# Kernel tuning notes

Hardware: AMD Instinct MI355X
Metric: run time of the kernel (lower is better)

The kernel has to match this reference:

```python
import jax, jax.numpy as jnp
import numpy as np

B, S, D = 8, 1024, 768
H = 12
DH = D // H  # 64


def setup_inputs() -> dict:
    key = jax.random.key(0)
    k1, k2 = jax.random.split(key)
    x = jax.random.normal(k1, (B, S, D), dtype=jnp.float32)
    attention_mask = jnp.zeros((B, 1, 1, S), dtype=jnp.float32)
    W = jax.random.normal(k2, (D, D), dtype=jnp.float32) * (1.0 / np.sqrt(D))
    b = jnp.zeros((D,), dtype=jnp.float32)
    return {"x": x, "attention_mask": attention_mask, "W": W, "b": b}


def reference(x, attention_mask, W, b):
    # Linear projection (torch Linear: y = x @ W^T + b; here W is [out,in])
    mixed = jnp.einsum('bsd,ed->bse', x, W) + b            # [B,S,D]
    # split heads -> [B,H,S,DH]
    xl = mixed.reshape(B, S, H, DH).transpose(0, 2, 1, 3)
    # self-attention with Q=K=V=xl
    scores = jnp.einsum('bhsd,bhtd->bhst', xl, xl) / jnp.sqrt(
        jnp.asarray(DH, dtype=xl.dtype))                    # [B,H,S,S]
    scores = scores + attention_mask
    probs = jax.nn.softmax(scores, axis=-1)
    ctx = jnp.einsum('bhst,bhtd->bhsd', probs, xl)          # [B,H,S,DH]
    ctx = ctx.transpose(0, 2, 1, 3).reshape(B, S, D)        # [B,S,D]
    return ctx
```

## Files before the change

### kernel.cpp

```cpp
#include <hip/hip_runtime.h>
#include <hip/hip_bf16.h>


#define D_MODEL 768
#define SEQ     1024
#define NHEAD   12
#define DHEAD   64
#define BATCH   8
#define QB      128
#define LOG2E   1.44269504088896f
#define FMLOG   28.8539008178f
#define SCLC    (0.125f * LOG2E)

typedef __attribute__((ext_vector_type(8)))  short bf16x8;
typedef __attribute__((ext_vector_type(4)))  short short4v;
typedef __attribute__((ext_vector_type(4)))  float f32x4;
typedef __attribute__((ext_vector_type(16))) float f32x16;

__device__ __forceinline__ unsigned short f2bf(float f) {
  __hip_bfloat16 h = __float2bfloat16(f);
  return *reinterpret_cast<unsigned short*>(&h);
}

__device__ __forceinline__ float fexp2(float x) {
#if __has_builtin(__builtin_amdgcn_exp2f)
  return __builtin_amdgcn_exp2f(x);
#else
  return exp2f(x);
#endif
}

__device__ __forceinline__ int lswz(int r, int c) {
  return (r << 6) + (c ^ ((r & 7) << 3));
}
__device__ __forceinline__ int tau(int t) {
  return (t & ~0xC) | ((t & 8) >> 1) | ((t & 4) << 1);
}

template<bool WRITE_T>
__global__ __launch_bounds__(256) void proj_kernel(
    const float* __restrict__ X, const float* __restrict__ W,
    const float* __restrict__ bias, unsigned short* __restrict__ mixed,
    unsigned short* __restrict__ mixedT)
{
  __shared__ unsigned short As[128][40];
  __shared__ unsigned short Bs[128][40];

  const int tid = threadIdx.x;
  const int l   = tid & 63;
  const int w   = tid >> 6;
  const int m0  = blockIdx.x * 128;
  const int n0  = blockIdx.y * 128;
  const int wm  = (w >> 1) * 64;
  const int wn  = (w & 1) * 64;
  const int lr  = l & 15;
  const int g   = l >> 4;
  const int lk  = g * 8;

  f32x4 acc[4][4] = {};

  for (int k0 = 0; k0 < D_MODEL; k0 += 32) {
    #pragma unroll
    for (int rr = 0; rr < 4; ++rr) {
      int p   = tid + rr * 256;
      int row = p >> 3;
      int cg  = (p & 7) * 4;
      f32x4 a  = *(const f32x4*)&X[(size_t)(m0 + row) * D_MODEL + k0 + cg];
      f32x4 bv = *(const f32x4*)&W[(size_t)(n0 + row) * D_MODEL + k0 + cg];
      short4v ap, bp;
      #pragma unroll
      for (int jj = 0; jj < 4; ++jj) { ap[jj] = (short)f2bf(a[jj]); bp[jj] = (short)f2bf(bv[jj]); }
      *(short4v*)&As[row][cg] = ap;
      *(short4v*)&Bs[row][cg] = bp;
    }
    __syncthreads();

    bf16x8 af[4], bfr[4];
    #pragma unroll
    for (int am = 0; am < 4; ++am) af[am]  = *(const bf16x8*)&As[wm + am * 16 + lr][lk];
    #pragma unroll
    for (int bn = 0; bn < 4; ++bn) bfr[bn] = *(const bf16x8*)&Bs[wn + bn * 16 + lr][lk];

    #pragma unroll
    for (int am = 0; am < 4; ++am)
      #pragma unroll
      for (int bn = 0; bn < 4; ++bn)
        acc[am][bn] = __builtin_amdgcn_mfma_f32_16x16x32_bf16(
            af[am], bfr[bn], acc[am][bn], 0, 0, 0);
    __syncthreads();
  }

  const int orow = g * 4;
  const int bT   = m0 >> 10;
  const int tl0  = (m0 & 1023) + wm + orow;
  #pragma unroll
  for (int bn = 0; bn < 4; ++bn) {
    int   col  = n0 + wn + bn * 16 + lr;
    float bcol = bias[col];
    size_t tbase = ((size_t)bT * D_MODEL + col) * SEQ;
    #pragma unroll
    for (int am = 0; am < 4; ++am) {
      short4v pk;
      #pragma unroll
      for (int i = 0; i < 4; ++i) {
        float v = acc[am][bn][i] + bcol;
        unsigned short hv = f2bf(v);
        mixed[(size_t)(m0 + wm + am * 16 + orow + i) * D_MODEL + col] = hv;
        pk[i] = (short)hv;
      }
      if (WRITE_T)
        *(short4v*)&mixedT[tbase + tau(tl0 + am * 16)] = pk;
    }
  }
}

template<bool PRE_T>
__global__ __launch_bounds__(256, 4) void attn_kernel(
    const unsigned short* __restrict__ mixed,
    const unsigned short* __restrict__ mixedT,
    const float* __restrict__ mask, float* __restrict__ out)
{
  __shared__ unsigned short Xbuf[2][4096];
  __shared__ unsigned short Tbuf[2][4096];
  __shared__ float maskE[SEQ];
  __shared__ float lb[128];
  __shared__ int   mflag;

  const int tid = threadIdx.x;
  const int l   = tid & 63;
  const int wq  = tid >> 6;
  const int l31 = l & 31;
  const int lh  = l >> 5;
  const int h4  = lh * 4;
  const int h8  = lh * 8;

  const int id  = blockIdx.x;
  const int xcd = id & 7;
  const int j   = id >> 3;
  const int pr  = xcd * 12 + (j >> 3);
  const int q0  = (j & 7) * QB;
  const int hd  = pr % NHEAD;
  const int b   = pr / NHEAD;

  const size_t base  = ((size_t)b * SEQ) * D_MODEL + hd * DHEAD;
  const size_t baseT = ((size_t)b * D_MODEL + hd * DHEAD) * SEQ;

  const int r0 = tid >> 3;
  const int sc = (tid & 7) * 8;

  if (tid == 0) mflag = 0;
  __syncthreads();
  {
    f32x4 mv = *(const f32x4*)&mask[(size_t)b * SEQ + tid * 4];
    #pragma unroll
    for (int jj = 0; jj < 4; ++jj)
      maskE[tid * 4 + jj] = fmaf(mv[jj], LOG2E, -FMLOG);
    if (mv[0] != 0.f || mv[1] != 0.f || mv[2] != 0.f || mv[3] != 0.f)
      mflag = 1;
  }

  unsigned short* QQ = &Xbuf[0][0];
  #pragma unroll
  for (int pp = 0; pp < 4; ++pp) {
    int g   = tid + pp * 256;
    int row = g >> 3;
    int c   = (g & 7) * 8;
    *(bf16x8*)&QQ[lswz(row, c)] =
        *(const bf16x8*)&mixed[base + (size_t)(q0 + row) * D_MODEL + c];
  }
  __syncthreads();

  const bool hm = (mflag != 0);
  bf16x8 qf[4];
  #pragma unroll
  for (int db = 0; db < 4; ++db)
    qf[db] = *(const bf16x8*)&QQ[lswz(wq * 32 + l31, db * 16 + h8)];
  __syncthreads();

  bf16x8 k0r, k1r, t0r, t1r;
  auto loadKV = [&](int tt) {
    k0r = *(const bf16x8*)&mixed[base + (size_t)(tt + r0) * D_MODEL + sc];
    k1r = *(const bf16x8*)&mixed[base + (size_t)(tt + r0 + 32) * D_MODEL + sc];
    if (PRE_T) {
      t0r = *(const bf16x8*)&mixedT[baseT + (size_t)r0 * SEQ + tt + sc];
      t1r = *(const bf16x8*)&mixedT[baseT + (size_t)(r0 + 32) * SEQ + tt + sc];
    }
  };
  auto stageKV = [&](unsigned short* Xd, unsigned short* Td) {
    *(bf16x8*)&Xd[lswz(r0, sc)]      = k0r;
    *(bf16x8*)&Xd[lswz(r0 + 32, sc)] = k1r;
    if (PRE_T) {
      *(bf16x8*)&Td[lswz(r0, sc)]      = t0r;
      *(bf16x8*)&Td[lswz(r0 + 32, sc)] = t1r;
    } else {
      int tl0 = tau(r0), tl1 = tau(r0 + 32);
      #pragma unroll
      for (int jj = 0; jj < 8; ++jj) {
        Td[lswz(sc + jj, tl0)] = (unsigned short)k0r[jj];
        Td[lswz(sc + jj, tl1)] = (unsigned short)k1r[jj];
      }
    }
  };

  unsigned short* Xc = &Xbuf[0][0];
  unsigned short* Xn = &Xbuf[1][0];
  unsigned short* Tc = &Tbuf[0][0];
  unsigned short* Tn = &Tbuf[1][0];

  loadKV(0);
  stageKV(Xc, Tc);
  __syncthreads();

  f32x16 c0 = {}, c1 = {};
  float lsum = 0.f;

  for (int t0 = 0; t0 < SEQ; t0 += 64) {
    const bool more = (t0 + 64 < SEQ);
    if (more) loadKV(t0 + 64);

    #pragma unroll
    for (int sub = 0; sub < 2; ++sub) {
      const int sr = sub * 32;

      f32x16 s = {};
      #pragma unroll
      for (int db = 0; db < 4; ++db) {
        bf16x8 kf = *(const bf16x8*)&Xc[lswz(sr + l31, db * 16 + h8)];
        s = __builtin_amdgcn_mfma_f32_32x32x16_bf16(kf, qf[db], s, 0, 0, 0);
      }

      float p[16];
      if (hm) {
        #pragma unroll
        for (int r = 0; r < 16; ++r) {
          int kvr = (r & 3) + 8 * (r >> 2) + h4;
          p[r] = fexp2(fmaf(s[r], SCLC, maskE[t0 + sr + kvr]));
          lsum += p[r];
        }
      } else {
        #pragma unroll
        for (int r = 0; r < 16; ++r) {
          p[r] = fexp2(fmaf(s[r], SCLC, -FMLOG));
          lsum += p[r];
        }
      }

      #pragma unroll
      for (int f = 0; f < 2; ++f) {
        bf16x8 pa;
        #pragma unroll
        for (int jj = 0; jj < 8; ++jj) pa[jj] = (short)f2bf(p[8 * f + jj]);
        const int cc = sr + f * 16 + h8;
        bf16x8 v0 = *(const bf16x8*)&Tc[lswz(l31, cc)];
        bf16x8 v1 = *(const bf16x8*)&Tc[lswz(32 + l31, cc)];
        c0 = __builtin_amdgcn_mfma_f32_32x32x16_bf16(pa, v0, c0, 0, 0, 0);
        c1 = __builtin_amdgcn_mfma_f32_32x32x16_bf16(pa, v1, c1, 0, 0, 0);
      }
    }

    if (more) {
      stageKV(Xn, Tn);
      __syncthreads();
    }
    unsigned short* t;
    t = Xc; Xc = Xn; Xn = t;
    t = Tc; Tc = Tn; Tn = t;
  }

  float l_tot = lsum + __shfl_xor(lsum, 32);
  if (lh == 0) lb[wq * 32 + l31] = l_tot;

  #pragma unroll
  for (int r = 0; r < 16; ++r) {
    int qr = (r & 3) + 8 * (r >> 2) + h4;
    float linv = __builtin_amdgcn_rcpf(lb[wq * 32 + qr]);
    int row = q0 + wq * 32 + qr;
    float* orow = &out[((size_t)b * SEQ + row) * D_MODEL + hd * DHEAD];
    orow[l31]      = c0[r] * linv;
    orow[32 + l31] = c1[r] * linv;
  }
}

extern "C" void kernel_launch(void* const* d_in, const int* in_sizes, int n_in,
                              void* d_out, int out_size, void* d_ws, size_t ws_size,
                              hipStream_t stream) {
  const float* x    = (const float*)d_in[0];
  const float* mask = (const float*)d_in[1];
  const float* W    = (const float*)d_in[2];
  const float* bias = (const float*)d_in[3];
  float* out        = (float*)d_out;

  const size_t NM = (size_t)8192 * D_MODEL;
  unsigned short* mixed  = (unsigned short*)d_ws;
  unsigned short* mixedT = mixed + NM;
  const size_t need = NM * 2 * 2;
  const bool preT = ws_size >= need;

  dim3 gp(8192 / 128, D_MODEL / 128);
  const int nblk = (SEQ / QB) * NHEAD * BATCH;

  if (preT) {
    proj_kernel<true><<<gp, 256, 0, stream>>>(x, W, bias, mixed, mixedT);
    attn_kernel<true><<<nblk, 256, 0, stream>>>(mixed, mixedT, mask, out);
  } else {
    proj_kernel<false><<<gp, 256, 0, stream>>>(x, W, bias, mixed, mixed);
    attn_kernel<false><<<nblk, 256, 0, stream>>>(mixed, mixed, mask, out);
  }
}
```

Measured before the change: 74.10 us.

## Double-buffer projection GEMM with register prefetch and halve M tile

The projection kernel now prefetches the next K-slab of X and W into registers while the MFMAs run on the current shared-memory buffer, then converts and stages it into the other of two LDS buffers, so each iteration needs one barrier instead of two. The M tile shrinks from 128 to 64 rows, which doubles the grid to 768 blocks to fill more CUs and lowers per-thread accumulator registers. The trade-off is less reuse of each W tile (W is reloaded twice as often) and more registers held for the prefetched slab.

```diff
diff --git a/kernel.cpp b/kernel.cpp
--- a/kernel.cpp
+++ b/kernel.cpp
@@ -43,51 +43,86 @@
     const float* __restrict__ bias, unsigned short* __restrict__ mixed,
     unsigned short* __restrict__ mixedT)
 {
-  __shared__ unsigned short As[128][40];
-  __shared__ unsigned short Bs[128][40];
+  __shared__ unsigned short As[2][64 * 40];
+  __shared__ unsigned short Bs[2][128 * 40];
 
   const int tid = threadIdx.x;
   const int l   = tid & 63;
   const int w   = tid >> 6;
-  const int m0  = blockIdx.x * 128;
+  const int m0  = blockIdx.x * 64;
   const int n0  = blockIdx.y * 128;
-  const int wm  = (w >> 1) * 64;
+  const int wm  = (w >> 1) * 32;
   const int wn  = (w & 1) * 64;
   const int lr  = l & 15;
   const int g   = l >> 4;
   const int lk  = g * 8;
 
-  f32x4 acc[4][4] = {};
-
+  const int ar = tid >> 2;
+  const int ac = (tid & 3) * 8;
+
+  f32x4 a0, a1, b0[2], b1[2];
+  auto loadSlab = [&](int k0) {
+    const float* pa = &X[(size_t)(m0 + ar) * D_MODEL + k0 + ac];
+    a0 = *(const f32x4*)pa;
+    a1 = *(const f32x4*)(pa + 4);
+    #pragma unroll
+    for (int p = 0; p < 2; ++p) {
+      const float* pb = &W[(size_t)(n0 + ar + p * 64) * D_MODEL + k0 + ac];
+      b0[p] = *(const f32x4*)pb;
+      b1[p] = *(const f32x4*)(pb + 4);
+    }
+  };
+  auto stageSlab = [&](int bb) {
+    bf16x8 av;
+    #pragma unroll
+    for (int jj = 0; jj < 4; ++jj) {
+      av[jj]     = (short)f2bf(a0[jj]);
+      av[4 + jj] = (short)f2bf(a1[jj]);
+    }
+    *(bf16x8*)&As[bb][ar * 40 + ac] = av;
+    #pragma unroll
+    for (int p = 0; p < 2; ++p) {
+      bf16x8 bv;
+      #pragma unroll
+      for (int jj = 0; jj < 4; ++jj) {
+        bv[jj]     = (short)f2bf(b0[p][jj]);
+        bv[4 + jj] = (short)f2bf(b1[p][jj]);
+      }
+      *(bf16x8*)&Bs[bb][(ar + p * 64) * 40 + ac] = bv;
+    }
+  };
+
+  f32x4 acc[2][4] = {};
+
+  loadSlab(0);
+  stageSlab(0);
+  __syncthreads();
+
+  int cur = 0;
   for (int k0 = 0; k0 < D_MODEL; k0 += 32) {
-    #pragma unroll
-    for (int rr = 0; rr < 4; ++rr) {
-      int p   = tid + rr * 256;
-      int row = p >> 3;
-      int cg  = (p & 7) * 4;
-      f32x4 a  = *(const f32x4*)&X[(size_t)(m0 + row) * D_MODEL + k0 + cg];
-      f32x4 bv = *(const f32x4*)&W[(size_t)(n0 + row) * D_MODEL + k0 + cg];
-      short4v ap, bp;
-      #pragma unroll
-      for (int jj = 0; jj < 4; ++jj) { ap[jj] = (short)f2bf(a[jj]); bp[jj] = (short)f2bf(bv[jj]); }
-      *(short4v*)&As[row][cg] = ap;
-      *(short4v*)&Bs[row][cg] = bp;
-    }
-    __syncthreads();
-
-    bf16x8 af[4], bfr[4];
-    #pragma unroll
-    for (int am = 0; am < 4; ++am) af[am]  = *(const bf16x8*)&As[wm + am * 16 + lr][lk];
-    #pragma unroll
-    for (int bn = 0; bn < 4; ++bn) bfr[bn] = *(const bf16x8*)&Bs[wn + bn * 16 + lr][lk];
-
-    #pragma unroll
-    for (int am = 0; am < 4; ++am)
+    const bool more = (k0 + 32 < D_MODEL);
+    if (more) loadSlab(k0 + 32);
+
+    bf16x8 af[2], bfr[4];
+    #pragma unroll
+    for (int am = 0; am < 2; ++am)
+      af[am]  = *(const bf16x8*)&As[cur][(wm + am * 16 + lr) * 40 + lk];
+    #pragma unroll
+    for (int bn = 0; bn < 4; ++bn)
+      bfr[bn] = *(const bf16x8*)&Bs[cur][(wn + bn * 16 + lr) * 40 + lk];
+
+    #pragma unroll
+    for (int am = 0; am < 2; ++am)
       #pragma unroll
       for (int bn = 0; bn < 4; ++bn)
         acc[am][bn] = __builtin_amdgcn_mfma_f32_16x16x32_bf16(
             af[am], bfr[bn], acc[am][bn], 0, 0, 0);
-    __syncthreads();
+
+    if (more) {
+      stageSlab(cur ^ 1);
+      __syncthreads();
+    }
+    cur ^= 1;
   }
 
   const int orow = g * 4;
@@ -99,7 +134,7 @@
     float bcol = bias[col];
     size_t tbase = ((size_t)bT * D_MODEL + col) * SEQ;
     #pragma unroll
-    for (int am = 0; am < 4; ++am) {
+    for (int am = 0; am < 2; ++am) {
       short4v pk;
       #pragma unroll
       for (int i = 0; i < 4; ++i) {
@@ -296,7 +331,7 @@
   const size_t need = NM * 2 * 2;
   const bool preT = ws_size >= need;
 
-  dim3 gp(8192 / 128, D_MODEL / 128);
+  dim3 gp(8192 / 64, D_MODEL / 128);
   const int nblk = (SEQ / QB) * NHEAD * BATCH;
 
   if (preT) {
```

Result: faster. 67.41 us (-9.0%).
